# Kernel tuning notes

Measured on AMD Instinct MI355X. Metric: run time of the kernel, lower is better.

The kernel has to match this reference:

```python
import jax, jax.numpy as jnp
import numpy as np

INPUT_SIZE = 8
WINDOW = 128
HIDDEN = 256
B, T = 1024, 256

def _cell(W_ih, W_hh, b_ih, b_hh, h, c, x):
    # PyTorch LSTM gate order: i, f, g, o
    gates = x @ W_ih.T + h @ W_hh.T + b_ih + b_hh  # [B, 4H]
    i, f, g, o = jnp.split(gates, 4, axis=-1)
    c = jax.nn.sigmoid(f) * c + jax.nn.sigmoid(i) * jnp.tanh(g)
    h = jax.nn.sigmoid(o) * jnp.tanh(c)
    return h, c

def setup_inputs() -> dict:
    key = jax.random.key(0)
    ks = jax.random.split(key, 12)
    s = 1.0 / np.sqrt(HIDDEN)
    u = lambda k, shape: jax.random.uniform(k, shape, jnp.float32, -s, s)
    return {
        'x': jax.random.normal(ks[0], (B, T, INPUT_SIZE), jnp.float32),
        'W_ih0': u(ks[1], (4 * HIDDEN, INPUT_SIZE)),
        'W_hh0': u(ks[2], (4 * HIDDEN, HIDDEN)),
        'b_ih0': u(ks[3], (4 * HIDDEN,)),
        'b_hh0': u(ks[4], (4 * HIDDEN,)),
        'W_ih1': u(ks[5], (4 * HIDDEN, HIDDEN)),
        'W_hh1': u(ks[6], (4 * HIDDEN, HIDDEN)),
        'b_ih1': u(ks[7], (4 * HIDDEN,)),
        'b_hh1': u(ks[8], (4 * HIDDEN,)),
        'W_lin': u(ks[9], (1, HIDDEN)),
        'b_lin': u(ks[10], (1,)),
    }

def reference(x, W_ih0, W_hh0, b_ih0, b_hh0, W_ih1, W_hh1, b_ih1, b_hh1, W_lin, b_lin):
    Bx = x.shape[0]
    h0 = jnp.zeros((Bx, HIDDEN), x.dtype)
    params = [(W_ih0, W_hh0, b_ih0, b_hh0), (W_ih1, W_hh1, b_ih1, b_hh1)]

    # ---- warmup: multi-layer LSTM over first WINDOW steps ----
    x_pre = jnp.swapaxes(x[:, :WINDOW], 0, 1)   # [W, B, in]
    x_post = jnp.swapaxes(x[:, WINDOW:, 1:], 0, 1)  # [T-W, B, in-1]

    hs, cs = [], []
    seq = x_pre
    for (Wi, Wh, bi, bh) in params:
        def step(carry, xt, Wi=Wi, Wh=Wh, bi=bi, bh=bh):
            h, c = carry
            h, c = _cell(Wi, Wh, bi, bh, h, c, xt)
            return (h, c), h
        (hT, cT), seq = jax.lax.scan(step, (h0, h0), seq)
        hs.append(hT); cs.append(cT)

    pred0 = hs[-1] @ W_lin.T + b_lin  # [B, 1]

    def ar_step(carry, xt_rest):
        h0_, c0_, h1_, c1_, pred = carry
        xin = jnp.concatenate([pred, xt_rest], axis=1)  # [B, in]
        h0_, c0_ = _cell(W_ih0, W_hh0, b_ih0, b_hh0, h0_, c0_, xin)
        h1_, c1_ = _cell(W_ih1, W_hh1, b_ih1, b_hh1, h1_, c1_, h0_)
        pred = h1_ @ W_lin.T + b_lin
        return (h0_, c0_, h1_, c1_, pred), pred

    carry0 = (hs[0], cs[0], hs[1], cs[1], pred0)
    _, preds = jax.lax.scan(ar_step, carry0, x_post)  # [T-W, B, 1]

    out = jnp.concatenate([pred0[None], preds], axis=0)  # [T-W+1, B, 1]
    return jnp.swapaxes(out, 0, 1)  # [B, T-W+1, 1]
```

## Files before the change

### kernel.cpp

```cpp
#include <hip/hip_runtime.h>
#include <cstdint>

#define HID  256
#define NG   1024
#define TT   256
#define WIN  128
#define K0   264
#define K1   512
#define OUTW 129

__device__ __forceinline__ float sigm(float z)  { return 1.0f / (1.0f + __expf(-z)); }
__device__ __forceinline__ float tanhx(float z) { float e = __expf(2.0f * z); return 1.0f - 2.0f / (e + 1.0f); }

__global__ void prep_kernel(const float* __restrict__ Wih0, const float* __restrict__ Whh0,
                            const float* __restrict__ bih0, const float* __restrict__ bhh0,
                            const float* __restrict__ Wih1, const float* __restrict__ Whh1,
                            const float* __restrict__ bih1, const float* __restrict__ bhh1,
                            float* __restrict__ ws) {
  const int n0 = K0 * NG, n1 = K1 * NG;
  const int total = n0 + n1 + 2 * NG;
  for (int i = blockIdx.x * blockDim.x + threadIdx.x; i < total; i += gridDim.x * blockDim.x) {
    float v;
    if (i < n0) {
      int k = i >> 10, g = i & (NG - 1);
      v = (k < 8) ? Wih0[g * 8 + k] : Whh0[g * HID + (k - 8)];
    } else if (i < n0 + n1) {
      int j = i - n0;
      int k = j >> 10, g = j & (NG - 1);
      v = (k < HID) ? Wih1[g * HID + k] : Whh1[g * HID + (k - HID)];
    } else if (i < n0 + n1 + NG) {
      int g = i - n0 - n1;
      v = bih0[g] + bhh0[g];
    } else {
      int g = i - n0 - n1 - NG;
      v = bih1[g] + bhh1[g];
    }
    ws[i] = v;
  }
}

__global__ __launch_bounds__(256) void lstm_ar_kernel(
    const float* __restrict__ x, const float* __restrict__ Wlin,
    const float* __restrict__ blin, const float* __restrict__ ws,
    float* __restrict__ out)
{
  const float* __restrict__ WT0 = ws;
  const float* __restrict__ WT1 = ws + K0 * NG;
  const float* __restrict__ bs0 = ws + (K0 + K1) * NG;
  const float* __restrict__ bs1 = bs0 + NG;

  __shared__ float in0[K0][4];
  __shared__ float in1[K1][4];
  __shared__ float c0s[HID][4];
  __shared__ float c1s[HID][4];
  __shared__ float gl[4][NG];
  __shared__ float predl[4];

  const int tid = threadIdx.x;
  const int r0  = blockIdx.x << 2;

  {
    float4 z = make_float4(0.f, 0.f, 0.f, 0.f);
    *(float4*)&c0s[tid][0]       = z;
    *(float4*)&c1s[tid][0]       = z;
    *(float4*)&in0[8 + tid][0]   = z;
    *(float4*)&in1[tid][0]       = z;
    *(float4*)&in1[HID + tid][0] = z;
  }
  __syncthreads();

  for (int t = 0; t < TT; ++t) {
    if (tid < 32) {
      int r = tid >> 3, k = tid & 7;
      float v;
      if (t >= WIN && k == 0) v = predl[r];
      else v = x[((size_t)(r0 + r) * TT + t) * 8 + k];
      in0[k][r] = v;
    }
    __syncthreads();

    {
      const int g4 = tid << 2;
      float4 b = *(const float4*)&bs0[g4];
      float4 a0 = b, a1 = b, a2 = b, a3 = b;
      #pragma unroll 4
      for (int k = 0; k < K0; ++k) {
        const float4 w = *(const float4*)&WT0[(k << 10) + g4];
        const float4 h = *(const float4*)&in0[k][0];
        a0.x += w.x * h.x; a0.y += w.y * h.x; a0.z += w.z * h.x; a0.w += w.w * h.x;
        a1.x += w.x * h.y; a1.y += w.y * h.y; a1.z += w.z * h.y; a1.w += w.w * h.y;
        a2.x += w.x * h.z; a2.y += w.y * h.z; a2.z += w.z * h.z; a2.w += w.w * h.z;
        a3.x += w.x * h.w; a3.y += w.y * h.w; a3.z += w.z * h.w; a3.w += w.w * h.w;
      }
      *(float4*)&gl[0][g4] = a0;
      *(float4*)&gl[1][g4] = a1;
      *(float4*)&gl[2][g4] = a2;
      *(float4*)&gl[3][g4] = a3;
    }
    __syncthreads();

    {
      const int j = tid;
      float4 c = *(const float4*)&c0s[j][0];
      float cc[4] = {c.x, c.y, c.z, c.w};
      float hh[4];
      #pragma unroll
      for (int r = 0; r < 4; ++r) {
        float ig = sigm(gl[r][j]);
        float fg = sigm(gl[r][HID + j]);
        float gg = tanhx(gl[r][2 * HID + j]);
        float og = sigm(gl[r][3 * HID + j]);
        float cn = fg * cc[r] + ig * gg;
        cc[r] = cn;
        hh[r] = og * tanhx(cn);
      }
      *(float4*)&c0s[j][0] = make_float4(cc[0], cc[1], cc[2], cc[3]);
      float4 hv = make_float4(hh[0], hh[1], hh[2], hh[3]);
      *(float4*)&in0[8 + j][0] = hv;
      *(float4*)&in1[j][0]     = hv;
    }
    __syncthreads();

    {
      const int g4 = tid << 2;
      float4 b = *(const float4*)&bs1[g4];
      float4 a0 = b, a1 = b, a2 = b, a3 = b;
      #pragma unroll 4
      for (int k = 0; k < K1; ++k) {
        const float4 w = *(const float4*)&WT1[(k << 10) + g4];
        const float4 h = *(const float4*)&in1[k][0];
        a0.x += w.x * h.x; a0.y += w.y * h.x; a0.z += w.z * h.x; a0.w += w.w * h.x;
        a1.x += w.x * h.y; a1.y += w.y * h.y; a1.z += w.z * h.y; a1.w += w.w * h.y;
        a2.x += w.x * h.z; a2.y += w.y * h.z; a2.z += w.z * h.z; a2.w += w.w * h.z;
        a3.x += w.x * h.w; a3.y += w.y * h.w; a3.z += w.z * h.w; a3.w += w.w * h.w;
      }
      *(float4*)&gl[0][g4] = a0;
      *(float4*)&gl[1][g4] = a1;
      *(float4*)&gl[2][g4] = a2;
      *(float4*)&gl[3][g4] = a3;
    }
    __syncthreads();

    {
      const int j = tid;
      float4 c = *(const float4*)&c1s[j][0];
      float cc[4] = {c.x, c.y, c.z, c.w};
      float hh[4];
      #pragma unroll
      for (int r = 0; r < 4; ++r) {
        float ig = sigm(gl[r][j]);
        float fg = sigm(gl[r][HID + j]);
        float gg = tanhx(gl[r][2 * HID + j]);
        float og = sigm(gl[r][3 * HID + j]);
        float cn = fg * cc[r] + ig * gg;
        cc[r] = cn;
        hh[r] = og * tanhx(cn);
      }
      *(float4*)&c1s[j][0] = make_float4(cc[0], cc[1], cc[2], cc[3]);
      *(float4*)&in1[HID + j][0] = make_float4(hh[0], hh[1], hh[2], hh[3]);
    }
    __syncthreads();

    if (t >= WIN - 1) {
      const int w = tid >> 6, l = tid & 63;
      float s = 0.f;
      #pragma unroll
      for (int q = 0; q < 4; ++q) {
        int j = l + (q << 6);
        s += Wlin[j] * in1[HID + j][w];
      }
      #pragma unroll
      for (int off = 32; off; off >>= 1) s += __shfl_down(s, off);
      if (l == 0) {
        float p = s + blin[0];
        predl[w] = p;
        out[(size_t)(r0 + w) * OUTW + (t - (WIN - 1))] = p;
      }
    }
    __syncthreads();
  }
}

extern "C" void kernel_launch(void* const* d_in, const int* in_sizes, int n_in,
                              void* d_out, int out_size, void* d_ws, size_t ws_size,
                              hipStream_t stream) {
  (void)in_sizes; (void)n_in; (void)out_size; (void)ws_size;
  const float* x    = (const float*)d_in[0];
  const float* Wih0 = (const float*)d_in[1];
  const float* Whh0 = (const float*)d_in[2];
  const float* bih0 = (const float*)d_in[3];
  const float* bhh0 = (const float*)d_in[4];
  const float* Wih1 = (const float*)d_in[5];
  const float* Whh1 = (const float*)d_in[6];
  const float* bih1 = (const float*)d_in[7];
  const float* bhh1 = (const float*)d_in[8];
  const float* Wlin = (const float*)d_in[9];
  const float* blin = (const float*)d_in[10];
  float* ws  = (float*)d_ws;
  float* out = (float*)d_out;

  prep_kernel<<<256, 256, 0, stream>>>(Wih0, Whh0, bih0, bhh0,
                                       Wih1, Whh1, bih1, bhh1, ws);
  lstm_ar_kernel<<<256, 256, 0, stream>>>(x, Wlin, blin, ws, out);
}
```

Measured before the change: 10.38 ms.

## Split hidden units across cooperative block clusters with weights resident in LDS

Adds a cooperative kernel where 8 clusters of 32 blocks each handle 128 batch rows. Each block keeps its 8-hidden-unit slice of both layers' weights in shared memory, and the hidden states are exchanged through double-buffered global memory with atomic-counter cluster barriers. The old kernel streamed all weights from global or L2 every timestep, and the new layout is meant to remove that weight traffic. The cost is two inter-block barriers per timestep, hidden-state reads from global, and a dependence on every block being co-resident. It falls back to the old kernel when the workspace is too small.

```diff
diff --git a/kernel.cpp b/kernel.cpp
--- a/kernel.cpp
+++ b/kernel.cpp
@@ -1,24 +1,53 @@
 #include <hip/hip_runtime.h>
 #include <cstdint>
 
-#define HID  256
-#define NG   1024
-#define TT   256
-#define WIN  128
-#define K0   264
-#define K1   512
+#define HID 256
+#define NG 1024
+#define TT 256
+#define WIN 128
+#define K0 264
+#define K1 512
 #define OUTW 129
+#define NCLUS 8
+#define CPC 32
+#define RPC 128
+#define NTHR 512
+
+#define OFF_WT0 0
+#define SZ_WT0 (K0*NG)
+#define OFF_WT1 (OFF_WT0+SZ_WT0)
+#define SZ_WT1 (K1*NG)
+#define OFF_BS0 (OFF_WT1+SZ_WT1)
+#define OFF_BS1 (OFF_BS0+NG)
+#define OFF_H0  (OFF_BS1+NG)
+#define SZ_H    (NCLUS*2*HID*RPC)
+#define OFF_H1  (OFF_H0+SZ_H)
+#define OFF_CTR (OFF_H1+SZ_H)
+#define WS_FLOATS (OFF_CTR+64)
+
+#define L_WL0  0
+#define L_WL1  (L_WL0 + K0*36)
+#define L_GL   (L_WL1 + K1*36)
+#define L_XIN  (L_GL + RPC*36)
+#define L_WLIN (L_XIN + 8*132)
+#define L_BS0  (L_WLIN + HID)
+#define L_BS1  (L_BS0 + 32)
+#define SMEM_FLOATS (L_BS1 + 32)
+#define SMEM_BYTES  (SMEM_FLOATS*4)
 
 __device__ __forceinline__ float sigm(float z)  { return 1.0f / (1.0f + __expf(-z)); }
 __device__ __forceinline__ float tanhx(float z) { float e = __expf(2.0f * z); return 1.0f - 2.0f / (e + 1.0f); }
+
+#define FMA4(A, W, S) { (A).x = fmaf((W).x,(S),(A).x); (A).y = fmaf((W).y,(S),(A).y); \
+                        (A).z = fmaf((W).z,(S),(A).z); (A).w = fmaf((W).w,(S),(A).w); }
 
 __global__ void prep_kernel(const float* __restrict__ Wih0, const float* __restrict__ Whh0,
                             const float* __restrict__ bih0, const float* __restrict__ bhh0,
                             const float* __restrict__ Wih1, const float* __restrict__ Whh1,
                             const float* __restrict__ bih1, const float* __restrict__ bhh1,
-                            float* __restrict__ ws) {
+                            float* __restrict__ ws, int full) {
   const int n0 = K0 * NG, n1 = K1 * NG;
-  const int total = n0 + n1 + 2 * NG;
+  const int total = full ? WS_FLOATS : (n0 + n1 + 2 * NG);
   for (int i = blockIdx.x * blockDim.x + threadIdx.x; i < total; i += gridDim.x * blockDim.x) {
     float v;
     if (i < n0) {
@@ -31,11 +60,221 @@
     } else if (i < n0 + n1 + NG) {
       int g = i - n0 - n1;
       v = bih0[g] + bhh0[g];
-    } else {
+    } else if (i < n0 + n1 + 2 * NG) {
       int g = i - n0 - n1 - NG;
       v = bih1[g] + bhh1[g];
+    } else {
+      v = 0.0f;
     }
     ws[i] = v;
+  }
+}
+
+__device__ __forceinline__ void reduce_store(float4 (&acc)[8], float* sGl, int rb, int g4, int ksl) {
+  #pragma unroll
+  for (int m = 0; m < 8; ++m) {
+    acc[m].x += __shfl_xor(acc[m].x, 16); acc[m].x += __shfl_xor(acc[m].x, 32);
+    acc[m].y += __shfl_xor(acc[m].y, 16); acc[m].y += __shfl_xor(acc[m].y, 32);
+    acc[m].z += __shfl_xor(acc[m].z, 16); acc[m].z += __shfl_xor(acc[m].z, 32);
+    acc[m].w += __shfl_xor(acc[m].w, 16); acc[m].w += __shfl_xor(acc[m].w, 32);
+  }
+  if (ksl == 0) {
+    #pragma unroll
+    for (int m = 0; m < 8; ++m) *(float4*)&sGl[(rb + m) * 36 + (g4 << 2)] = acc[m];
+  }
+}
+
+__device__ __forceinline__ void epilogue(const float* sGl, const float* sBs, float (&cst)[2],
+                                         float* hdst, int jl, int rr) {
+  #pragma unroll
+  for (int q = 0; q < 2; ++q) {
+    const int r = (rr << 1) + q;
+    const float gi = sGl[r * 36 +      jl] + sBs[jl];
+    const float gf = sGl[r * 36 +  8 + jl] + sBs[8 + jl];
+    const float gg = sGl[r * 36 + 16 + jl] + sBs[16 + jl];
+    const float go = sGl[r * 36 + 24 + jl] + sBs[24 + jl];
+    float c = sigm(gf) * cst[q] + sigm(gi) * tanhx(gg);
+    cst[q] = c;
+    hdst[r] = sigm(go) * tanhx(c);
+  }
+}
+
+__device__ __forceinline__ void cluster_barrier(unsigned int* ctr, unsigned int target) {
+  __threadfence();
+  __syncthreads();
+  if (threadIdx.x == 0) {
+    __hip_atomic_fetch_add(ctr, 1u, __ATOMIC_RELEASE, __HIP_MEMORY_SCOPE_AGENT);
+    while (__hip_atomic_load(ctr, __ATOMIC_RELAXED, __HIP_MEMORY_SCOPE_AGENT) < target)
+      __builtin_amdgcn_s_sleep(4);
+  }
+  __syncthreads();
+  (void)__hip_atomic_load(ctr, __ATOMIC_ACQUIRE, __HIP_MEMORY_SCOPE_AGENT);
+}
+
+__global__ __launch_bounds__(NTHR) void lstm_cluster(
+    const float* __restrict__ x, const float* __restrict__ Wlin,
+    const float* __restrict__ blin, float* __restrict__ ws,
+    float* __restrict__ out)
+{
+  extern __shared__ float sm[];
+  float* sWL0  = sm + L_WL0;
+  float* sWL1  = sm + L_WL1;
+  float* sGl   = sm + L_GL;
+  float* sXin  = sm + L_XIN;
+  float* sWlin = sm + L_WLIN;
+  float* sBs0  = sm + L_BS0;
+  float* sBs1  = sm + L_BS1;
+
+  const int clus = blockIdx.x & 7;
+  const int cu   = blockIdx.x >> 3;
+  const int tid  = threadIdx.x;
+  const int lane = tid & 63;
+  const int wave = tid >> 6;
+  const int ksl  = lane >> 4;
+  const int t16  = lane & 15;
+  const int tile = wave * 16 + t16;
+  const int g4   = tile & 7;
+  const int rb   = (tile >> 3) * 8;
+  const int jl   = tid & 7;
+  const int rr   = tid >> 3;
+  const int kc   = tid & 3;
+  const int rp   = tid >> 2;
+  unsigned int* ctr = (unsigned int*)(ws + OFF_CTR) + clus;
+
+  for (int idx = tid; idx < K0 * 32; idx += NTHR) {
+    int k = idx >> 5, g = idx & 31;
+    sWL0[k * 36 + g] = ws[OFF_WT0 + k * NG + (g >> 3) * HID + cu * 8 + (g & 7)];
+  }
+  for (int idx = tid; idx < K1 * 32; idx += NTHR) {
+    int k = idx >> 5, g = idx & 31;
+    sWL1[k * 36 + g] = ws[OFF_WT1 + k * NG + (g >> 3) * HID + cu * 8 + (g & 7)];
+  }
+  if (tid < HID) sWlin[tid] = Wlin[tid];
+  if (tid < 32) {
+    sBs0[tid] = ws[OFF_BS0 + (tid >> 3) * HID + cu * 8 + (tid & 7)];
+    sBs1[tid] = ws[OFF_BS1 + (tid >> 3) * HID + cu * 8 + (tid & 7)];
+  }
+  const float blv = blin[0];
+  float c0q[2] = {0.f, 0.f}, c1q[2] = {0.f, 0.f};
+  unsigned int barSeq = 0;
+  __syncthreads();
+
+  for (int t = 0; t < TT; ++t) {
+    const int p = t & 1;
+    float* h0prev = ws + OFF_H0 + (size_t)(clus * 2 + p) * HID * RPC;
+    float* h0new  = ws + OFF_H0 + (size_t)(clus * 2 + (p ^ 1)) * HID * RPC;
+    float* h1prev = ws + OFF_H1 + (size_t)(clus * 2 + p) * HID * RPC;
+    float* h1new  = ws + OFF_H1 + (size_t)(clus * 2 + (p ^ 1)) * HID * RPC;
+
+    {
+      const int f = tid & 7;
+      #pragma unroll
+      for (int q = 0; q < 2; ++q) {
+        const int r = ((tid >> 3) << 1) + q;
+        if (f > 0 || t < WIN)
+          sXin[f * 132 + r] = x[((size_t)(clus * RPC + r) * TT + t) * 8 + f];
+      }
+    }
+    if (t >= WIN) {
+      float s0 = 0.f, s1 = 0.f, s2 = 0.f, s3 = 0.f;
+      const float* hp = h1prev + rp;
+      #pragma unroll 4
+      for (int i = 0; i < 64; i += 4) {
+        const int k = (kc << 6) + i;
+        s0 = fmaf(sWlin[k],     hp[(size_t)k * RPC],            s0);
+        s1 = fmaf(sWlin[k + 1], hp[(size_t)(k + 1) * RPC],      s1);
+        s2 = fmaf(sWlin[k + 2], hp[(size_t)(k + 2) * RPC],      s2);
+        s3 = fmaf(sWlin[k + 3], hp[(size_t)(k + 3) * RPC],      s3);
+      }
+      float s = (s0 + s1) + (s2 + s3);
+      s += __shfl_xor(s, 1);
+      s += __shfl_xor(s, 2);
+      if (kc == 0) {
+        const float pv = s + blv;
+        sXin[rp] = pv;
+        if (cu == 0) out[(size_t)(clus * RPC + rp) * OUTW + (t - WIN)] = pv;
+      }
+    }
+    __syncthreads();
+
+    {
+      float4 acc[8];
+      #pragma unroll
+      for (int m = 0; m < 8; ++m) acc[m] = make_float4(0.f, 0.f, 0.f, 0.f);
+      #pragma unroll
+      for (int i = 0; i < 2; ++i) {
+        const int k = (i << 2) + ksl;
+        const float4 w  = *(const float4*)&sWL0[k * 36 + (g4 << 2)];
+        const float4 ha = *(const float4*)&sXin[k * 132 + rb];
+        const float4 hb = *(const float4*)&sXin[k * 132 + rb + 4];
+        FMA4(acc[0], w, ha.x); FMA4(acc[1], w, ha.y); FMA4(acc[2], w, ha.z); FMA4(acc[3], w, ha.w);
+        FMA4(acc[4], w, hb.x); FMA4(acc[5], w, hb.y); FMA4(acc[6], w, hb.z); FMA4(acc[7], w, hb.w);
+      }
+      #pragma unroll 4
+      for (int i = 2; i < 66; ++i) {
+        const int k = (i << 2) + ksl;
+        const float4 w  = *(const float4*)&sWL0[k * 36 + (g4 << 2)];
+        const float* hp = h0prev + (size_t)(k - 8) * RPC + rb;
+        const float4 ha = *(const float4*)hp;
+        const float4 hb = *(const float4*)(hp + 4);
+        FMA4(acc[0], w, ha.x); FMA4(acc[1], w, ha.y); FMA4(acc[2], w, ha.z); FMA4(acc[3], w, ha.w);
+        FMA4(acc[4], w, hb.x); FMA4(acc[5], w, hb.y); FMA4(acc[6], w, hb.z); FMA4(acc[7], w, hb.w);
+      }
+      reduce_store(acc, sGl, rb, g4, ksl);
+    }
+    __syncthreads();
+
+    epilogue(sGl, sBs0, c0q, h0new + (size_t)(cu * 8 + jl) * RPC, jl, rr);
+    cluster_barrier(ctr, CPC * (++barSeq));
+
+    {
+      float4 acc[8];
+      #pragma unroll
+      for (int m = 0; m < 8; ++m) acc[m] = make_float4(0.f, 0.f, 0.f, 0.f);
+      #pragma unroll 4
+      for (int i = 0; i < 64; ++i) {
+        const int k = (i << 2) + ksl;
+        const float4 w  = *(const float4*)&sWL1[k * 36 + (g4 << 2)];
+        const float* hp = h0new + (size_t)k * RPC + rb;
+        const float4 ha = *(const float4*)hp;
+        const float4 hb = *(const float4*)(hp + 4);
+        FMA4(acc[0], w, ha.x); FMA4(acc[1], w, ha.y); FMA4(acc[2], w, ha.z); FMA4(acc[3], w, ha.w);
+        FMA4(acc[4], w, hb.x); FMA4(acc[5], w, hb.y); FMA4(acc[6], w, hb.z); FMA4(acc[7], w, hb.w);
+      }
+      #pragma unroll 4
+      for (int i = 64; i < 128; ++i) {
+        const int k = (i << 2) + ksl;
+        const float4 w  = *(const float4*)&sWL1[k * 36 + (g4 << 2)];
+        const float* hp = h1prev + (size_t)(k - 256) * RPC + rb;
+        const float4 ha = *(const float4*)hp;
+        const float4 hb = *(const float4*)(hp + 4);
+        FMA4(acc[0], w, ha.x); FMA4(acc[1], w, ha.y); FMA4(acc[2], w, ha.z); FMA4(acc[3], w, ha.w);
+        FMA4(acc[4], w, hb.x); FMA4(acc[5], w, hb.y); FMA4(acc[6], w, hb.z); FMA4(acc[7], w, hb.w);
+      }
+      reduce_store(acc, sGl, rb, g4, ksl);
+    }
+    __syncthreads();
+
+    epilogue(sGl, sBs1, c1q, h1new + (size_t)(cu * 8 + jl) * RPC, jl, rr);
+    cluster_barrier(ctr, CPC * (++barSeq));
+  }
+
+  if (cu == 0) {
+    const float* h1f = ws + OFF_H1 + (size_t)(clus * 2 + 0) * HID * RPC;
+    float s0 = 0.f, s1 = 0.f, s2 = 0.f, s3 = 0.f;
+    const float* hp = h1f + rp;
+    #pragma unroll 4
+    for (int i = 0; i < 64; i += 4) {
+      const int k = (kc << 6) + i;
+      s0 = fmaf(sWlin[k],     hp[(size_t)k * RPC],       s0);
+      s1 = fmaf(sWlin[k + 1], hp[(size_t)(k + 1) * RPC], s1);
+      s2 = fmaf(sWlin[k + 2], hp[(size_t)(k + 2) * RPC], s2);
+      s3 = fmaf(sWlin[k + 3], hp[(size_t)(k + 3) * RPC], s3);
+    }
+    float s = (s0 + s1) + (s2 + s3);
+    s += __shfl_xor(s, 1);
+    s += __shfl_xor(s, 2);
+    if (kc == 0) out[(size_t)(clus * RPC + rp) * OUTW + 128] = s + blv;
   }
 }
 
@@ -44,10 +283,10 @@
     const float* __restrict__ blin, const float* __restrict__ ws,
     float* __restrict__ out)
 {
-  const float* __restrict__ WT0 = ws;
-  const float* __restrict__ WT1 = ws + K0 * NG;
-  const float* __restrict__ bs0 = ws + (K0 + K1) * NG;
-  const float* __restrict__ bs1 = bs0 + NG;
+  const float* WT0 = ws;
+  const float* WT1 = ws + K0 * NG;
+  const float* bs0 = ws + (K0 + K1) * NG;
+  const float* bs1 = bs0 + NG;
 
   __shared__ float in0[K0][4];
   __shared__ float in1[K1][4];
@@ -78,7 +317,6 @@
       in0[k][r] = v;
     }
     __syncthreads();
-
     {
       const int g4 = tid << 2;
       float4 b = *(const float4*)&bs0[g4];
@@ -87,18 +325,15 @@
       for (int k = 0; k < K0; ++k) {
         const float4 w = *(const float4*)&WT0[(k << 10) + g4];
         const float4 h = *(const float4*)&in0[k][0];
-        a0.x += w.x * h.x; a0.y += w.y * h.x; a0.z += w.z * h.x; a0.w += w.w * h.x;
-        a1.x += w.x * h.y; a1.y += w.y * h.y; a1.z += w.z * h.y; a1.w += w.w * h.y;
-        a2.x += w.x * h.z; a2.y += w.y * h.z; a2.z += w.z * h.z; a2.w += w.w * h.z;
-        a3.x += w.x * h.w; a3.y += w.y * h.w; a3.z += w.z * h.w; a3.w += w.w * h.w;
-      }
-      *(float4*)&gl[0][g4] = a0;
-      *(float4*)&gl[1][g4] = a1;
-      *(float4*)&gl[2][g4] = a2;
-      *(float4*)&gl[3][g4] = a3;
-    }
-    __syncthreads();
-
+        a0.x += w.x*h.x; a0.y += w.y*h.x; a0.z += w.z*h.x; a0.w += w.w*h.x;
+        a1.x += w.x*h.y; a1.y += w.y*h.y; a1.z += w.z*h.y; a1.w += w.w*h.y;
+        a2.x += w.x*h.z; a2.y += w.y*h.z; a2.z += w.z*h.z; a2.w += w.w*h.z;
+        a3.x += w.x*h.w; a3.y += w.y*h.w; a3.z += w.z*h.w; a3.w += w.w*h.w;
+      }
+      *(float4*)&gl[0][g4] = a0; *(float4*)&gl[1][g4] = a1;
+      *(float4*)&gl[2][g4] = a2; *(float4*)&gl[3][g4] = a3;
+    }
+    __syncthreads();
     {
       const int j = tid;
       float4 c = *(const float4*)&c0s[j][0];
@@ -111,8 +346,7 @@
         float gg = tanhx(gl[r][2 * HID + j]);
         float og = sigm(gl[r][3 * HID + j]);
         float cn = fg * cc[r] + ig * gg;
-        cc[r] = cn;
-        hh[r] = og * tanhx(cn);
+        cc[r] = cn; hh[r] = og * tanhx(cn);
       }
       *(float4*)&c0s[j][0] = make_float4(cc[0], cc[1], cc[2], cc[3]);
       float4 hv = make_float4(hh[0], hh[1], hh[2], hh[3]);
@@ -120,7 +354,6 @@
       *(float4*)&in1[j][0]     = hv;
     }
     __syncthreads();
-
     {
       const int g4 = tid << 2;
       float4 b = *(const float4*)&bs1[g4];
@@ -129,18 +362,15 @@
       for (int k = 0; k < K1; ++k) {
         const float4 w = *(const float4*)&WT1[(k << 10) + g4];
         const float4 h = *(const float4*)&in1[k][0];
-        a0.x += w.x * h.x; a0.y += w.y * h.x; a0.z += w.z * h.x; a0.w += w.w * h.x;
-        a1.x += w.x * h.y; a1.y += w.y * h.y; a1.z += w.z * h.y; a1.w += w.w * h.y;
-        a2.x += w.x * h.z; a2.y += w.y * h.z; a2.z += w.z * h.z; a2.w += w.w * h.z;
-        a3.x += w.x * h.w; a3.y += w.y * h.w; a3.z += w.z * h.w; a3.w += w.w * h.w;
-      }
-      *(float4*)&gl[0][g4] = a0;
-      *(float4*)&gl[1][g4] = a1;
-      *(float4*)&gl[2][g4] = a2;
-      *(float4*)&gl[3][g4] = a3;
-    }
-    __syncthreads();
-
+        a0.x += w.x*h.x; a0.y += w.y*h.x; a0.z += w.z*h.x; a0.w += w.w*h.x;
+        a1.x += w.x*h.y; a1.y += w.y*h.y; a1.z += w.z*h.y; a1.w += w.w*h.y;
+        a2.x += w.x*h.z; a2.y += w.y*h.z; a2.z += w.z*h.z; a2.w += w.w*h.z;
+        a3.x += w.x*h.w; a3.y += w.y*h.w; a3.z += w.z*h.w; a3.w += w.w*h.w;
+      }
+      *(float4*)&gl[0][g4] = a0; *(float4*)&gl[1][g4] = a1;
+      *(float4*)&gl[2][g4] = a2; *(float4*)&gl[3][g4] = a3;
+    }
+    __syncthreads();
     {
       const int j = tid;
       float4 c = *(const float4*)&c1s[j][0];
@@ -153,14 +383,12 @@
         float gg = tanhx(gl[r][2 * HID + j]);
         float og = sigm(gl[r][3 * HID + j]);
         float cn = fg * cc[r] + ig * gg;
-        cc[r] = cn;
-        hh[r] = og * tanhx(cn);
+        cc[r] = cn; hh[r] = og * tanhx(cn);
       }
       *(float4*)&c1s[j][0] = make_float4(cc[0], cc[1], cc[2], cc[3]);
       *(float4*)&in1[HID + j][0] = make_float4(hh[0], hh[1], hh[2], hh[3]);
     }
     __syncthreads();
-
     if (t >= WIN - 1) {
       const int w = tid >> 6, l = tid & 63;
       float s = 0.f;
@@ -172,9 +400,9 @@
       #pragma unroll
       for (int off = 32; off; off >>= 1) s += __shfl_down(s, off);
       if (l == 0) {
-        float p = s + blin[0];
-        predl[w] = p;
-        out[(size_t)(r0 + w) * OUTW + (t - (WIN - 1))] = p;
+        float pv = s + blin[0];
+        predl[w] = pv;
+        out[(size_t)(r0 + w) * OUTW + (t - (WIN - 1))] = pv;
       }
     }
     __syncthreads();
@@ -184,7 +412,7 @@
 extern "C" void kernel_launch(void* const* d_in, const int* in_sizes, int n_in,
                               void* d_out, int out_size, void* d_ws, size_t ws_size,
                               hipStream_t stream) {
-  (void)in_sizes; (void)n_in; (void)out_size; (void)ws_size;
+  (void)in_sizes; (void)n_in; (void)out_size;
   const float* x    = (const float*)d_in[0];
   const float* Wih0 = (const float*)d_in[1];
   const float* Whh0 = (const float*)d_in[2];
@@ -199,7 +427,18 @@
   float* ws  = (float*)d_ws;
   float* out = (float*)d_out;
 
-  prep_kernel<<<256, 256, 0, stream>>>(Wih0, Whh0, bih0, bhh0,
-                                       Wih1, Whh1, bih1, bhh1, ws);
-  lstm_ar_kernel<<<256, 256, 0, stream>>>(x, Wlin, blin, ws, out);
-}
+  const int full = (ws_size >= (size_t)WS_FLOATS * sizeof(float)) ? 1 : 0;
+  prep_kernel<<<1024, 256, 0, stream>>>(Wih0, Whh0, bih0, bhh0,
+                                        Wih1, Whh1, bih1, bhh1, ws, full);
+  if (full) {
+    (void)hipFuncSetAttribute(reinterpret_cast<const void*>(lstm_cluster),
+                              hipFuncAttributeMaxDynamicSharedMemorySize, SMEM_BYTES);
+    const float* xp = x; const float* wl = Wlin; const float* bl = blin;
+    float* wsp = ws; float* op = out;
+    void* args[] = {(void*)&xp, (void*)&wl, (void*)&bl, (void*)&wsp, (void*)&op};
+    (void)hipLaunchCooperativeKernel(reinterpret_cast<const void*>(lstm_cluster),
+                                     dim3(NCLUS * CPC), dim3(NTHR), args, SMEM_BYTES, stream);
+  } else {
+    lstm_ar_kernel<<<256, 256, 0, stream>>>(x, Wlin, blin, ws, out);
+  }
+}
```

Result: slower. 36.98 ms (+256.1%).
